# Optimization experiments

Measured on AMD Instinct MI355X. Metric: run time of the kernel, lower is better.

## Reference

```python
import jax, jax.numpy as jnp
import numpy as np

B, LC, LP, D, H = 16, 1024, 1024, 128, 4
PFEAT = 1024  # hardcoded p_param rows in the original module


def _xavier(k, shape, gain=1.414):
    fan_in, fan_out = shape[-2], shape[-1]
    a = gain * np.sqrt(6.0 / (fan_in + fan_out))
    return jax.random.uniform(k, shape, minval=-a, maxval=a, dtype=jnp.float32)


def setup_inputs() -> dict:
    key = jax.random.key(0)
    ks = jax.random.split(key, 24)
    inp = {
        "c": jax.random.normal(ks[0], (B, LC, 1), dtype=jnp.float32),
        "c_mask": jnp.ones((B, LC), dtype=jnp.float32),
        "p": jax.random.normal(ks[1], (B, LP, PFEAT), dtype=jnp.float32),
        "p_mask": jnp.ones((B, LP), dtype=jnp.float32),
        # learned params; linear weights stored as [in, out] (transposed vs torch)
        "c_param": _xavier(ks[2], (1, D)),
        "p_param": _xavier(ks[3], (PFEAT, D)),
        "U": _xavier(ks[4], (H, D, D)),
        "W_p2c": _xavier(ks[5], (H, D, D)),
        "b_p2c": jnp.zeros((H, D), dtype=jnp.float32),
        "W_c2p": _xavier(ks[6], (H, D, D)),
        "b_c2p": jnp.zeros((H, D), dtype=jnp.float32),
        "Wh_c": _xavier(ks[7], (H, D, D)),
        "bh_c": jnp.zeros((H, D), dtype=jnp.float32),
        "Wh_p": _xavier(ks[8], (H, D, D)),
        "bh_p": jnp.zeros((H, D), dtype=jnp.float32),
        "Wa_c": _xavier(ks[9], (H, 2 * D, 1))[..., 0],  # [H, 2D]
        "ba_c": jnp.zeros((H,), dtype=jnp.float32),
        "Wa_p": _xavier(ks[10], (H, 2 * D, 1))[..., 0],
        "ba_p": jnp.zeros((H,), dtype=jnp.float32),
        "W_comb_c": _xavier(ks[11], (H * D, D)),
        "b_comb_c": jnp.zeros((D,), dtype=jnp.float32),
        "W_comb_p": _xavier(ks[12], (H * D, D)),
        "b_comb_p": jnp.zeros((D,), dtype=jnp.float32),
    }
    return inp


def _mask_softmax(a, mask):
    # a, mask broadcastable; softmax over last axis with mask applied post-exp
    a_max = jnp.max(a, axis=-1, keepdims=True)
    e = jnp.exp(a - a_max) * mask
    return e / (jnp.sum(e, axis=-1, keepdims=True) + 1e-6)


def reference(c, c_mask, p, p_mask, c_param, p_param, U, W_p2c, b_p2c,
              W_c2p, b_c2p, Wh_c, bh_c, Wh_p, bh_p, Wa_c, ba_c, Wa_p, ba_p,
              W_comb_c, b_comb_c, W_comb_p, b_comb_p):
    b = c.shape[0]
    cv = jnp.matmul(c, c_param)          # [b, Lc, d]
    pv = jnp.matmul(p, p_param)          # [b, Lp, d]

    # bilinear attention map per head: [b, H, Lc, Lp]
    A = jnp.tanh(jnp.einsum("bld,hde,bme->bhlm", cv, U, pv))
    A = A * (c_mask[:, None, :, None] * p_mask[:, None, None, :])

    pt = jnp.tanh(jnp.einsum("bmd,hde->bhme", pv, W_p2c) + b_p2c[None, :, None, :])
    c_trans = jnp.einsum("bhlm,bhme->bhle", A, pt)      # [b,H,Lc,d]
    ct = jnp.tanh(jnp.einsum("bld,hde->bhle", cv, W_c2p) + b_c2p[None, :, None, :])
    p_trans = jnp.einsum("bhlm,bhle->bhme", A, ct)      # [b,H,Lp,d]

    hc = jnp.tanh(jnp.einsum("bld,hde->bhle", cv, Wh_c) + bh_c[None, :, None, :])
    hp = jnp.tanh(jnp.einsum("bmd,hde->bhme", pv, Wh_p) + bh_p[None, :, None, :])

    # attention logits: linear over concat([hidden, trans]) -> split the weight
    score_c = (jnp.einsum("bhle,he->bhl", hc, Wa_c[:, :128])
               + jnp.einsum("bhle,he->bhl", c_trans, Wa_c[:, 128:])
               + ba_c[None, :, None])
    score_p = (jnp.einsum("bhme,he->bhm", hp, Wa_p[:, :128])
               + jnp.einsum("bhme,he->bhm", p_trans, Wa_p[:, 128:])
               + ba_p[None, :, None])

    c_att = _mask_softmax(score_c, c_mask[:, None, :])  # [b,H,Lc]
    p_att = _mask_softmax(score_p, p_mask[:, None, :])  # [b,H,Lp]

    cf = jnp.einsum("bld,bhl->bhd", cv, c_att).reshape(b, -1)  # [b, H*d]
    pf = jnp.einsum("bmd,bhm->bhd", pv, p_att).reshape(b, -1)

    cf_final = cf @ W_comb_c + b_comb_c  # [b, d]
    pf_final = pf @ W_comb_p + b_comb_p  # [b, d]
    return cf_final[:, :, None] * pf_final[:, None, :]  # [b, d, d]
```

## Files before the change

kernel.cpp:

```cpp
#include <hip/hip_runtime.h>


using bf16x8 = __attribute__((ext_vector_type(8))) short;
using u16x8  = __attribute__((ext_vector_type(8))) unsigned short;
using f32x4  = __attribute__((ext_vector_type(4))) float;

#define TWO_LOG2E 2.8853900817779268f

__device__ __forceinline__ float exp2_raw(float x){
#if __has_builtin(__builtin_amdgcn_exp2f)
  return __builtin_amdgcn_exp2f(x);
#else
  float r; asm("v_exp_f32 %0, %1" : "=v"(r) : "v"(x)); return r;
#endif
}
__device__ __forceinline__ float tanh_fast(float x){
  float e = exp2_raw(x * TWO_LOG2E);
  return fmaf(-2.0f, __builtin_amdgcn_rcpf(e + 1.0f), 1.0f);
}
__device__ __forceinline__ unsigned short f2bf(float f){
  unsigned u = __float_as_uint(f);
  u = (u + 0x7FFFu + ((u >> 16) & 1u)) >> 16;
  return (unsigned short)u;
}
__device__ __forceinline__ float bf2f(unsigned short s){
  return __uint_as_float((unsigned)s << 16);
}
__device__ __forceinline__ unsigned cvt_pk_bf16(float a, float b){
  unsigned r;
  asm("v_cvt_pk_bf16_f32 %0, %1, %2" : "=v"(r) : "v"(a), "v"(b));
  return r;
}
__device__ __forceinline__ void split8(const float4& x, const float4& y, bf16x8& hi, bf16x8& lo){
  unsigned h0 = cvt_pk_bf16(x.x, x.y);
  unsigned h1 = cvt_pk_bf16(x.z, x.w);
  unsigned h2 = cvt_pk_bf16(y.x, y.y);
  unsigned h3 = cvt_pk_bf16(y.z, y.w);
  float r0 = x.x - __uint_as_float(h0 << 16);
  float r1 = x.y - __uint_as_float(h0 & 0xffff0000u);
  float r2 = x.z - __uint_as_float(h1 << 16);
  float r3 = x.w - __uint_as_float(h1 & 0xffff0000u);
  float r4 = y.x - __uint_as_float(h2 << 16);
  float r5 = y.y - __uint_as_float(h2 & 0xffff0000u);
  float r6 = y.z - __uint_as_float(h3 << 16);
  float r7 = y.w - __uint_as_float(h3 & 0xffff0000u);
  uint4 H = make_uint4(h0, h1, h2, h3);
  uint4 L = make_uint4(cvt_pk_bf16(r0, r1), cvt_pk_bf16(r2, r3),
                       cvt_pk_bf16(r4, r5), cvt_pk_bf16(r6, r7));
  hi = __builtin_bit_cast(bf16x8, H);
  lo = __builtin_bit_cast(bf16x8, L);
}

__global__ __launch_bounds__(256) void ka_prep(
    const float* __restrict__ c_param,
    const float* __restrict__ U, const float* __restrict__ W_comb_c,
    const float* __restrict__ Wh_c, const float* __restrict__ W_c2p,
    const float* __restrict__ p_param, const float* __restrict__ W_p2c,
    const float* __restrict__ Wh_p,
    float* __restrict__ uh, float* __restrict__ wccv,
    float* __restrict__ whc_v, float* __restrict__ wc2p_v,
    unsigned short* __restrict__ ppT_hi, unsigned short* __restrict__ ppT_lo,
    unsigned short* __restrict__ wp2cT_hi, unsigned short* __restrict__ wp2cT_lo,
    unsigned short* __restrict__ whpT_hi, unsigned short* __restrict__ whpT_lo)
{
  __shared__ float T[64*68];
  int bid0 = blockIdx.x, t = threadIdx.x;
  if (bid0 < 4) {
    int h = bid0;
    if (t < 128) {
      float s_uh = 0.f, s_wcc = 0.f, s_whc = 0.f, s_wc2p = 0.f;
      for (int d = 0; d < 128; ++d) {
        float cp = c_param[d];
        s_uh   += cp * U[(h*128 + d)*128 + t];
        s_wcc  += cp * W_comb_c[(h*128 + d)*128 + t];
        s_whc  += cp * Wh_c[(h*128 + d)*128 + t];
        s_wc2p += cp * W_c2p[(h*128 + d)*128 + t];
      }
      uh[h*128 + t]     = s_uh;
      wccv[h*128 + t]   = s_wcc;
      whc_v[h*128 + t]  = s_whc;
      wc2p_v[h*128 + t] = s_wc2p;
    }
    return;
  }
  int bid = bid0 - 4;
  const float* src; unsigned short* dh; unsigned short* dl;
  int k0, e0, dpitch, drow0;
  if (bid < 32) {
    k0 = (bid >> 1)*64; e0 = (bid & 1)*64;
    src = p_param; dh = ppT_hi; dl = ppT_lo; dpitch = 1024; drow0 = e0;
  } else if (bid < 48) {
    int w = bid - 32; int h = w >> 2, ki = (w >> 1) & 1, ej = w & 1;
    k0 = ki*64; e0 = ej*64;
    src = W_p2c + h*16384; dh = wp2cT_hi; dl = wp2cT_lo; dpitch = 128;
    drow0 = h*128 + e0;
  } else {
    int w = bid - 48; int h = w >> 2, ki = (w >> 1) & 1, ej = w & 1;
    k0 = ki*64; e0 = ej*64;
    src = Wh_p + h*16384; dh = whpT_hi; dl = whpT_lo; dpitch = 128;
    drow0 = h*128 + e0;
  }
  {
    int r = t >> 2, cs = (t & 3)*4;
    const float* s = src + (k0 + r)*128 + e0 + cs;
    #pragma unroll
    for (int j = 0; j < 4; ++j) {
      float4 v = *(const float4*)(s + j*16);
      *(float4*)&T[r*68 + cs + j*16] = v;
    }
  }
  __syncthreads();
  {
    int e = t >> 2, ks = (t & 3)*16;
    unsigned short hs[16], ls[16];
    #pragma unroll
    for (int j = 0; j < 16; ++j) {
      float v = T[(ks + j)*68 + e];
      unsigned short hh = f2bf(v);
      hs[j] = hh; ls[j] = f2bf(v - bf2f(hh));
    }
    unsigned short* ph = dh + (drow0 + e)*dpitch + k0 + ks;
    unsigned short* pl = dl + (drow0 + e)*dpitch + k0 + ks;
    *(u16x8*)ph       = *(u16x8*)&hs[0];
    *(u16x8*)(ph + 8) = *(u16x8*)&hs[8];
    *(u16x8*)pl       = *(u16x8*)&ls[0];
    *(u16x8*)(pl + 8) = *(u16x8*)&ls[8];
  }
}

__global__ __launch_bounds__(256) void kb_pv_maps(
    const float* __restrict__ p,
    const unsigned short* __restrict__ ppT_hi, const unsigned short* __restrict__ ppT_lo,
    float* __restrict__ pv_part0, float* __restrict__ pv_part1,
    const float* __restrict__ c, const float* __restrict__ c_mask,
    const float* __restrict__ whc_v, const float* __restrict__ wc2p_v,
    const float* __restrict__ bh_c, const float* __restrict__ b_c2p,
    const float* __restrict__ Wa_c, const float* __restrict__ Wa_p,
    const float* __restrict__ ba_c,
    float* __restrict__ score_c, float2* __restrict__ pairP)
{
  __shared__ __align__(16) char smem[36864];
  int bid = blockIdx.x, t = threadIdx.x;
  if (bid < 512) {
    short* Bh = (short*)smem;
    short* Bl = (short*)(smem + 18432);
    int khalf = bid >> 8, rowtile = bid & 255;
    int kbase = khalf * 512;
    int row0 = rowtile * 64;
    float* __restrict__ pvp = khalf ? pv_part1 : pv_part0;
    int w = t >> 6, lane = t & 63;
    int l15 = lane & 15, l4 = lane >> 4;

    int bcol = t >> 1, bkh = (t & 1) * 32;
    const unsigned short* gBh = ppT_hi + bcol*1024 + kbase + bkh;
    const unsigned short* gBl = ppT_lo + bcol*1024 + kbase + bkh;
    short* sBh = &Bh[bcol*72 + bkh];
    short* sBl = &Bl[bcol*72 + bkh];

    const float* gA = p + (row0 + w*16 + l15)*1024 + kbase + l4*8;

    u16x8 rb[8];
    float4 ra[4];

    #pragma unroll
    for (int j = 0; j < 4; ++j) {
      rb[j]   = *(const u16x8*)(gBh + j*8);
      rb[4+j] = *(const u16x8*)(gBl + j*8);
    }
    #pragma unroll
    for (int j = 0; j < 4; ++j)
      ra[j] = *(const float4*)(gA + (j>>1)*32 + (j&1)*4);

    f32x4 acc[8];
    #pragma unroll
    for (int n = 0; n < 8; ++n) acc[n] = (f32x4){0.f,0.f,0.f,0.f};

    for (int kc = 0; kc < 8; ++kc) {
      __syncthreads();
      #pragma unroll
      for (int j = 0; j < 4; ++j) {
        *(u16x8*)(sBh + j*8) = rb[j];
        *(u16x8*)(sBl + j*8) = rb[4+j];
      }
      if (kc < 7) {
        #pragma unroll
        for (int j = 0; j < 4; ++j) {
          rb[j]   = *(const u16x8*)(gBh + (kc+1)*64 + j*8);
          rb[4+j] = *(const u16x8*)(gBl + (kc+1)*64 + j*8);
        }
      }
      float4 ran0, ran1, ran2, ran3;
      if (kc < 7) {
        const float* gAn = gA + (kc+1)*64;
        ran0 = *(const float4*)(gAn);
        ran1 = *(const float4*)(gAn + 4);
        ran2 = *(const float4*)(gAn + 32);
        ran3 = *(const float4*)(gAn + 36);
      }
      __syncthreads();
      #pragma unroll
      for (int ks = 0; ks < 2; ++ks) {
        bf16x8 ah, al;
        split8(ra[2*ks], ra[2*ks+1], ah, al);
        #pragma unroll
        for (int ct = 0; ct < 8; ++ct) {
          bf16x8 bh = *(const bf16x8*)&Bh[(ct*16 + l15)*72 + ks*32 + l4*8];
          bf16x8 bl = *(const bf16x8*)&Bl[(ct*16 + l15)*72 + ks*32 + l4*8];
          acc[ct] = __builtin_amdgcn_mfma_f32_16x16x32_bf16(ah, bh, acc[ct], 0, 0, 0);
          acc[ct] = __builtin_amdgcn_mfma_f32_16x16x32_bf16(ah, bl, acc[ct], 0, 0, 0);
          acc[ct] = __builtin_amdgcn_mfma_f32_16x16x32_bf16(al, bh, acc[ct], 0, 0, 0);
        }
      }
      if (kc < 7) { ra[0] = ran0; ra[1] = ran1; ra[2] = ran2; ra[3] = ran3; }
    }

    #pragma unroll
    for (int ct = 0; ct < 8; ++ct) {
      int col = ct*16 + l15;
      #pragma unroll
      for (int r = 0; r < 4; ++r) {
        int row = row0 + w*16 + l4*4 + r;
        pvp[row*128 + col] = acc[ct][r];
      }
    }
  } else {
    float* fsh = (float*)smem;
    float* whc_l  = fsh;
    float* wc2p_l = fsh + 128;
    float* bhc_l  = fsh + 256;
    float* bc2p_l = fsh + 384;
    float* wac1_l = fsh + 512;
    float* wap2_l = fsh + 640;
    int i = bid - 512;
    int b = i >> 4, h = (i >> 2) & 3, lc = i & 3;
    if (t < 128) {
      whc_l[t]  = whc_v[h*128 + t];
      wc2p_l[t] = wc2p_v[h*128 + t];
      bhc_l[t]  = bh_c[h*128 + t];
      bc2p_l[t] = b_c2p[h*128 + t];
      wac1_l[t] = Wa_c[h*256 + t];
      wap2_l[t] = Wa_p[h*256 + 128 + t];
    }
    __syncthreads();
    int l = lc*256 + t;
    float cl = c[b*1024 + l];
    float a1 = 0.f, a2 = 0.f;
    #pragma unroll 4
    for (int e = 0; e < 128; ++e) {
      a1 += wac1_l[e] * tanh_fast(cl*whc_l[e]  + bhc_l[e]);
      a2 += wap2_l[e] * tanh_fast(cl*wc2p_l[e] + bc2p_l[e]);
    }
    int o = (b*4 + h)*1024 + l;
    score_c[o] = a1 + ba_c[h];
    pairP[o] = make_float2(TWO_LOG2E * cl, c_mask[b*1024 + l] * a2);
  }
}

__global__ __launch_bounds__(256) void kc_head(
    const float* __restrict__ pv0, const float* __restrict__ pv1,
    const unsigned short* __restrict__ wp2cT_hi, const unsigned short* __restrict__ wp2cT_lo,
    const unsigned short* __restrict__ whpT_hi, const unsigned short* __restrict__ whpT_lo,
    const float* __restrict__ b_p2c, const float* __restrict__ bh_p,
    const float* __restrict__ Wa_c, const float* __restrict__ Wa_p,
    const float* __restrict__ p_mask, const float* __restrict__ ba_p,
    const float* __restrict__ uh,
    float2* __restrict__ pairC, float* __restrict__ score_p,
    float* __restrict__ g_arr, float* __restrict__ pv_sum)
{
  __shared__ __align__(16) short Whs[64*136];
  __shared__ __align__(16) short Wls[64*136];
  int t = threadIdx.x;
  int bid = blockIdx.x;
  int ph = bid >> 7, mtile = bid & 127;
  int path = ph >> 2, h = ph & 3;
  int w = t >> 6, lane = t & 63;
  int l15 = lane & 15, l4 = lane >> 4;

  const unsigned short* Wgh = (path ? whpT_hi : wp2cT_hi) + h*16384;
  const unsigned short* Wgl = (path ? whpT_lo : wp2cT_lo) + h*16384;
  int e2 = t >> 2, k0s = (t & 3)*32;

  u16x8 wr_h[4], wr_l[4];
  {
    const u16x8* sh = (const u16x8*)(Wgh + e2*128 + k0s);
    const u16x8* sl = (const u16x8*)(Wgl + e2*128 + k0s);
    #pragma unroll
    for (int j = 0; j < 4; ++j) { wr_h[j] = sh[j]; wr_l[j] = sl[j]; }
  }

  const float* bias_g = path ? bh_p : b_p2c;
  float biasv[8], wav[8];
  #pragma unroll
  for (int n = 0; n < 8; ++n) {
    int col = n*16 + l15;
    biasv[n] = bias_g[h*128 + col];
    wav[n]   = path ? Wa_p[h*256 + col] : Wa_c[h*256 + 128 + col];
  }

  int rowbase = mtile*128 + w*32;
  bf16x8 afh[2][4], afl[2][4];
  float gacc[2] = {0.f, 0.f};
  #pragma unroll
  for (int rtile = 0; rtile < 2; ++rtile) {
    int off = (rowbase + rtile*16 + l15)*128 + l4*8;
    #pragma unroll
    for (int kt = 0; kt < 4; ++kt) {
      float4 x0 = *(const float4*)(pv0 + off + kt*32);
      float4 y0 = *(const float4*)(pv0 + off + kt*32 + 4);
      float4 x1 = *(const float4*)(pv1 + off + kt*32);
      float4 y1 = *(const float4*)(pv1 + off + kt*32 + 4);
      float4 x = make_float4(x0.x+x1.x, x0.y+x1.y, x0.z+x1.z, x0.w+x1.w);
      float4 y = make_float4(y0.x+y1.x, y0.y+y1.y, y0.z+y1.z, y0.w+y1.w);
      if (ph == 0) {
        *(float4*)(pv_sum + off + kt*32)     = x;
        *(float4*)(pv_sum + off + kt*32 + 4) = y;
      }
      split8(x, y, afh[rtile][kt], afl[rtile][kt]);
      if (!path) {
        float4 u0 = *(const float4*)(uh + h*128 + kt*32 + l4*8);
        float4 u1 = *(const float4*)(uh + h*128 + kt*32 + l4*8 + 4);
        gacc[rtile] += x.x*u0.x + x.y*u0.y + x.z*u0.z + x.w*u0.w
                     + y.x*u1.x + y.y*u1.y + y.z*u1.z + y.w*u1.w;
      }
    }
  }
  if (!path) {
    #pragma unroll
    for (int rtile = 0; rtile < 2; ++rtile) {
      float gg = gacc[rtile];
      gg += __shfl_xor(gg, 16, 64);
      gg += __shfl_xor(gg, 32, 64);
      if (l4 == 0) {
        int grow = rowbase + rtile*16 + l15;
        int bb = grow >> 10, m = grow & 1023;
        int idx = (bb*4 + h)*1024 + m;
        g_arr[idx] = gg;
        pairC[idx].x = TWO_LOG2E * gg;
      }
    }
  }

  f32x4 acc[2][8];
  #pragma unroll
  for (int rtile = 0; rtile < 2; ++rtile)
    #pragma unroll
    for (int n = 0; n < 8; ++n) acc[rtile][n] = (f32x4){0.f,0.f,0.f,0.f};

  {
    u16x8* dhh = (u16x8*)&Whs[e2*136 + k0s];
    u16x8* dll = (u16x8*)&Wls[e2*136 + k0s];
    #pragma unroll
    for (int j = 0; j < 4; ++j) { dhh[j] = wr_h[j]; dll[j] = wr_l[j]; }
  }
  __syncthreads();

  {
    const u16x8* sh = (const u16x8*)(Wgh + (64 + e2)*128 + k0s);
    const u16x8* sl = (const u16x8*)(Wgl + (64 + e2)*128 + k0s);
    #pragma unroll
    for (int j = 0; j < 4; ++j) { wr_h[j] = sh[j]; wr_l[j] = sl[j]; }
  }

  #pragma unroll
  for (int n = 0; n < 4; ++n) {
    #pragma unroll
    for (int kt = 0; kt < 4; ++kt) {
      bf16x8 bh = *(const bf16x8*)&Whs[(n*16 + l15)*136 + kt*32 + l4*8];
      bf16x8 bl = *(const bf16x8*)&Wls[(n*16 + l15)*136 + kt*32 + l4*8];
      #pragma unroll
      for (int rtile = 0; rtile < 2; ++rtile) {
        acc[rtile][n] = __builtin_amdgcn_mfma_f32_16x16x32_bf16(afh[rtile][kt], bh, acc[rtile][n], 0, 0, 0);
        acc[rtile][n] = __builtin_amdgcn_mfma_f32_16x16x32_bf16(afh[rtile][kt], bl, acc[rtile][n], 0, 0, 0);
        acc[rtile][n] = __builtin_amdgcn_mfma_f32_16x16x32_bf16(afl[rtile][kt], bh, acc[rtile][n], 0, 0, 0);
      }
    }
  }
  __syncthreads();
  {
    u16x8* dhh = (u16x8*)&Whs[e2*136 + k0s];
    u16x8* dll = (u16x8*)&Wls[e2*136 + k0s];
    #pragma unroll
    for (int j = 0; j < 4; ++j) { dhh[j] = wr_h[j]; dll[j] = wr_l[j]; }
  }
  __syncthreads();
  #pragma unroll
  for (int n = 0; n < 4; ++n) {
    int nn = 4 + n;
    #pragma unroll
    for (int kt = 0; kt < 4; ++kt) {
      bf16x8 bh = *(const bf16x8*)&Whs[(n*16 + l15)*136 + kt*32 + l4*8];
      bf16x8 bl = *(const bf16x8*)&Wls[(n*16 + l15)*136 + kt*32 + l4*8];
      #pragma unroll
      for (int rtile = 0; rtile < 2; ++rtile) {
        acc[rtile][nn] = __builtin_amdgcn_mfma_f32_16x16x32_bf16(afh[rtile][kt], bh, acc[rtile][nn], 0, 0, 0);
        acc[rtile][nn] = __builtin_amdgcn_mfma_f32_16x16x32_bf16(afh[rtile][kt], bl, acc[rtile][nn], 0, 0, 0);
        acc[rtile][nn] = __builtin_amdgcn_mfma_f32_16x16x32_bf16(afl[rtile][kt], bh, acc[rtile][nn], 0, 0, 0);
      }
    }
  }

  #pragma unroll
  for (int rtile = 0; rtile < 2; ++rtile) {
    float pp0 = 0.f, pp1 = 0.f, pp2 = 0.f, pp3 = 0.f;
    #pragma unroll
    for (int n = 0; n < 8; ++n) {
      float bb = biasv[n], ww = wav[n];
      pp0 += ww * tanh_fast(acc[rtile][n][0] + bb);
      pp1 += ww * tanh_fast(acc[rtile][n][1] + bb);
      pp2 += ww * tanh_fast(acc[rtile][n][2] + bb);
      pp3 += ww * tanh_fast(acc[rtile][n][3] + bb);
    }
    #pragma unroll
    for (int off = 1; off < 16; off <<= 1) {
      pp0 += __shfl_xor(pp0, off, 64);
      pp1 += __shfl_xor(pp1, off, 64);
      pp2 += __shfl_xor(pp2, off, 64);
      pp3 += __shfl_xor(pp3, off, 64);
    }
    if (l15 == 0) {
      int grow = rowbase + rtile*16 + l4*4;
      int bb = grow >> 10, m = grow & 1023;
      int idx = (bb*4 + h)*1024 + m;
      if (path) {
        float bap = ba_p[h];
        *(float4*)&score_p[idx] = make_float4(pp0+bap, pp1+bap, pp2+bap, pp3+bap);
      } else {
        float4 mk = *(const float4*)&p_mask[bb*1024 + m];
        pairC[idx+0].y = mk.x * pp0;
        pairC[idx+1].y = mk.y * pp1;
        pairC[idx+2].y = mk.z * pp2;
        pairC[idx+3].y = mk.w * pp3;
      }
    }
  }
}

__global__ __launch_bounds__(256) void kd_scores(
    const float* __restrict__ c, const float* __restrict__ c_mask, const float* __restrict__ p_mask,
    const float* __restrict__ g_arr,
    const float2* __restrict__ pairC, const float2* __restrict__ pairP,
    float* __restrict__ score_c, float* __restrict__ score_p)
{
  __shared__ float2 pr[256];
  __shared__ float red[4];
  int bid = blockIdx.x, t = threadIdx.x;
  int side = bid >> 9;
  int r = bid & 511;
  int b = r >> 5, h = (r >> 3) & 3, ac = (r >> 2) & 1, jc = r & 3;
  int bh = b*4 + h;
  const float2* pair = (side ? pairP : pairC) + bh*1024 + jc*256;

  float2 mine = pair[t];
  pr[t] = mine;
  float partB = mine.y;
  #pragma unroll
  for (int off = 1; off < 64; off <<= 1) partB += __shfl_xor(partB, off, 64);
  if ((t & 63) == 0) red[t >> 6] = partB;

  int ai1 = ac*512 + t, ai2 = ai1 + 256;
  float alpha1, alpha2, mask1, mask2;
  if (side) {
    alpha1 = g_arr[bh*1024 + ai1]; alpha2 = g_arr[bh*1024 + ai2];
    mask1  = p_mask[b*1024 + ai1]; mask2  = p_mask[b*1024 + ai2];
  } else {
    alpha1 = c[b*1024 + ai1]; alpha2 = c[b*1024 + ai2];
    mask1  = c_mask[b*1024 + ai1]; mask2  = c_mask[b*1024 + ai2];
  }
  __syncthreads();
  float sB = red[0] + red[1] + red[2] + red[3];

  float acc1 = 0.f, acc2 = 0.f;
  #pragma unroll 8
  for (int j = 0; j < 256; ++j) {
    float2 gb = pr[j];
    float e1 = exp2_raw(alpha1 * gb.x);
    float e2 = exp2_raw(alpha2 * gb.x);
    acc1 = fmaf(gb.y, __builtin_amdgcn_rcpf(e1 + 1.0f), acc1);
    acc2 = fmaf(gb.y, __builtin_amdgcn_rcpf(e2 + 1.0f), acc2);
  }
  float* sc = side ? score_p : score_c;
  atomicAdd(sc + bh*1024 + ai1, mask1 * (sB - 2.0f*acc1));
  atomicAdd(sc + bh*1024 + ai2, mask2 * (sB - 2.0f*acc2));
}

__device__ __forceinline__ float blk_red_max(float v, float* red, int t){
  red[t] = v; __syncthreads();
  for (int s = 128; s; s >>= 1) { if (t < s) red[t] = fmaxf(red[t], red[t+s]); __syncthreads(); }
  float r = red[0]; __syncthreads();
  return r;
}
__device__ __forceinline__ float blk_red_sum(float v, float* red, int t){
  red[t] = v; __syncthreads();
  for (int s = 128; s; s >>= 1) { if (t < s) red[t] += red[t+s]; __syncthreads(); }
  float r = red[0]; __syncthreads();
  return r;
}

__global__ __launch_bounds__(256) void ke_soft(
    const float* __restrict__ c, const float* __restrict__ c_mask, const float* __restrict__ p_mask,
    const float* __restrict__ score_c, const float* __restrict__ score_p,
    const float* __restrict__ pv_sum,
    float* __restrict__ s_c, float* __restrict__ pf_pool)
{
  __shared__ float sv[1024];
  __shared__ float red[256];
  int bid = blockIdx.x, t = threadIdx.x;
  bool sideP = bid >= 64;
  int i = bid & 63;
  int b = i >> 2, h = i & 3, bh = b*4 + h;
  const float* sc = (sideP ? score_p : score_c) + bh*1024;
  const float* mk = (sideP ? p_mask : c_mask) + b*1024;

  float v[4];
  float mx = -1e30f;
  #pragma unroll
  for (int j = 0; j < 4; ++j) { v[j] = sc[t + j*256]; mx = fmaxf(mx, v[j]); }
  mx = blk_red_max(mx, red, t);
  float sum = 0.f;
  #pragma unroll
  for (int j = 0; j < 4; ++j) {
    float e = exp2_raw((v[j] - mx) * 1.4426950408889634f) * mk[t + j*256];
    sv[t + j*256] = e;
    sum += e;
  }
  sum = blk_red_sum(sum, red, t);
  float rinv = __fdividef(1.0f, sum + 1e-6f);

  if (!sideP) {
    float a = 0.f;
    #pragma unroll
    for (int j = 0; j < 4; ++j) a += sv[t + j*256] * rinv * c[b*1024 + t + j*256];
    a = blk_red_sum(a, red, t);
    if (t == 0) s_c[bh] = a;
  } else {
    #pragma unroll
    for (int j = 0; j < 4; ++j) sv[t + j*256] *= rinv;
    __syncthreads();
    int e = t & 127, half = t >> 7;
    float acc = 0.f;
    const float* base = pv_sum + (b*1024 + half*512)*128 + e;
    #pragma unroll 4
    for (int m = 0; m < 512; ++m) acc += sv[half*512 + m] * base[m*128];
    red[t] = acc; __syncthreads();
    if (t < 128) pf_pool[bh*128 + t] = red[t] + red[t + 128];
  }
}

__global__ __launch_bounds__(256) void kf_final(
    const float* __restrict__ s_c, const float* __restrict__ wccv,
    const float* __restrict__ b_comb_c, const float* __restrict__ pf_pool,
    const float* __restrict__ W_comb_p, const float* __restrict__ b_comb_p,
    float* __restrict__ out)
{
  __shared__ float pfr[512];
  __shared__ float cfl[128], pfl[128];
  int b = blockIdx.x, t = threadIdx.x;
  pfr[t]       = pf_pool[b*512 + t];
  pfr[t + 256] = pf_pool[b*512 + t + 256];
  __syncthreads();
  if (t < 128) {
    float cf = b_comb_c[t];
    #pragma unroll
    for (int h = 0; h < 4; ++h) cf += s_c[b*4 + h] * wccv[h*128 + t];
    float pf = b_comb_p[t];
    #pragma unroll 8
    for (int i = 0; i < 512; ++i) pf += pfr[i] * W_comb_p[i*128 + t];
    cfl[t] = cf; pfl[t] = pf;
  }
  __syncthreads();
  #pragma unroll
  for (int k = 0; k < 64; ++k) {
    int idx = k*256 + t;
    out[b*16384 + idx] = cfl[idx >> 7] * pfl[idx & 127];
  }
}

extern "C" void kernel_launch(void* const* d_in, const int* in_sizes, int n_in,
                              void* d_out, int out_size, void* d_ws, size_t ws_size,
                              hipStream_t stream)
{
  const float* c        = (const float*)d_in[0];
  const float* c_mask   = (const float*)d_in[1];
  const float* p        = (const float*)d_in[2];
  const float* p_mask   = (const float*)d_in[3];
  const float* c_param  = (const float*)d_in[4];
  const float* p_param  = (const float*)d_in[5];
  const float* U        = (const float*)d_in[6];
  const float* W_p2c    = (const float*)d_in[7];
  const float* b_p2c    = (const float*)d_in[8];
  const float* W_c2p    = (const float*)d_in[9];
  const float* b_c2p    = (const float*)d_in[10];
  const float* Wh_c     = (const float*)d_in[11];
  const float* bh_c     = (const float*)d_in[12];
  const float* Wh_p     = (const float*)d_in[13];
  const float* bh_p     = (const float*)d_in[14];
  const float* Wa_c     = (const float*)d_in[15];
  const float* ba_c     = (const float*)d_in[16];
  const float* Wa_p     = (const float*)d_in[17];
  const float* ba_p     = (const float*)d_in[18];
  const float* W_comb_c = (const float*)d_in[19];
  const float* b_comb_c = (const float*)d_in[20];
  const float* W_comb_p = (const float*)d_in[21];
  const float* b_comb_p = (const float*)d_in[22];
  float* out = (float*)d_out;

  char* ws = (char*)d_ws;
  float*          pv_part0 = (float*)         (ws + 0);
  float*          pv_part1 = (float*)         (ws + 8388608);
  float*          pv_sum   = (float*)         (ws + 16777216);
  unsigned short* ppT_hi   = (unsigned short*)(ws + 25165824);
  unsigned short* ppT_lo   = (unsigned short*)(ws + 25427968);
  unsigned short* wp2cT_hi = (unsigned short*)(ws + 25690112);
  unsigned short* wp2cT_lo = (unsigned short*)(ws + 25821184);
  unsigned short* whpT_hi  = (unsigned short*)(ws + 25952256);
  unsigned short* whpT_lo  = (unsigned short*)(ws + 26083328);
  float*          uh       = (float*)         (ws + 26214400);
  float*          wccv     = (float*)         (ws + 26216448);
  float*          whc_v    = (float*)         (ws + 26218496);
  float*          wc2p_v   = (float*)         (ws + 26220544);
  float*          g_arr    = (float*)         (ws + 26222592);
  float2*         pairC    = (float2*)        (ws + 26484736);
  float2*         pairP    = (float2*)        (ws + 27009024);
  float*          score_c  = (float*)         (ws + 27533312);
  float*          score_p  = (float*)         (ws + 27795456);
  float*          s_c      = (float*)         (ws + 28057600);
  float*          pf_pool  = (float*)         (ws + 28057856);

  ka_prep<<<dim3(68), dim3(256), 0, stream>>>(
      c_param, U, W_comb_c, Wh_c, W_c2p, p_param, W_p2c, Wh_p,
      uh, wccv, whc_v, wc2p_v,
      ppT_hi, ppT_lo, wp2cT_hi, wp2cT_lo, whpT_hi, whpT_lo);

  kb_pv_maps<<<dim3(768), dim3(256), 0, stream>>>(
      p, ppT_hi, ppT_lo, pv_part0, pv_part1,
      c, c_mask, whc_v, wc2p_v, bh_c, b_c2p, Wa_c, Wa_p, ba_c,
      score_c, pairP);

  kc_head<<<dim3(1024), dim3(256), 0, stream>>>(
      pv_part0, pv_part1, wp2cT_hi, wp2cT_lo, whpT_hi, whpT_lo,
      b_p2c, bh_p, Wa_c, Wa_p, p_mask, ba_p, uh, pairC, score_p, g_arr, pv_sum);

  kd_scores<<<dim3(1024), dim3(256), 0, stream>>>(
      c, c_mask, p_mask, g_arr, pairC, pairP, score_c, score_p);

  ke_soft<<<dim3(128), dim3(256), 0, stream>>>(
      c, c_mask, p_mask, score_c, score_p, pv_sum, s_c, pf_pool);

  kf_final<<<dim3(16), dim3(256), 0, stream>>>(
      s_c, wccv, b_comb_c, pf_pool, W_comb_p, b_comb_p, out);
}
```

Before: 150.5 us.

## Share tanh tiles between both score directions and split p-side pooling across blocks

```diff
diff --git a/kernel.cpp b/kernel.cpp
--- a/kernel.cpp
+++ b/kernel.cpp
@@ -436,51 +436,57 @@
 }
 
 __global__ __launch_bounds__(256) void kd_scores(
-    const float* __restrict__ c, const float* __restrict__ c_mask, const float* __restrict__ p_mask,
+    const float* __restrict__ c_mask, const float* __restrict__ p_mask,
     const float* __restrict__ g_arr,
     const float2* __restrict__ pairC, const float2* __restrict__ pairP,
     float* __restrict__ score_c, float* __restrict__ score_p)
 {
-  __shared__ float2 pr[256];
-  __shared__ float red[4];
+  __shared__ float T[128*65];
+  __shared__ float gm_s[64], ptw_s[64], pm_s[64];
+  __shared__ float kl_s[128], ctw_s[128], cm_s[128];
   int bid = blockIdx.x, t = threadIdx.x;
-  int side = bid >> 9;
-  int r = bid & 511;
-  int b = r >> 5, h = (r >> 3) & 3, ac = (r >> 2) & 1, jc = r & 3;
-  int bh = b*4 + h;
-  const float2* pair = (side ? pairP : pairC) + bh*1024 + jc*256;
-
-  float2 mine = pair[t];
-  pr[t] = mine;
-  float partB = mine.y;
-  #pragma unroll
-  for (int off = 1; off < 64; off <<= 1) partB += __shfl_xor(partB, off, 64);
-  if ((t & 63) == 0) red[t >> 6] = partB;
-
-  int ai1 = ac*512 + t, ai2 = ai1 + 256;
-  float alpha1, alpha2, mask1, mask2;
-  if (side) {
-    alpha1 = g_arr[bh*1024 + ai1]; alpha2 = g_arr[bh*1024 + ai2];
-    mask1  = p_mask[b*1024 + ai1]; mask2  = p_mask[b*1024 + ai2];
-  } else {
-    alpha1 = c[b*1024 + ai1]; alpha2 = c[b*1024 + ai2];
-    mask1  = c_mask[b*1024 + ai1]; mask2  = c_mask[b*1024 + ai2];
-  }
-  __syncthreads();
-  float sB = red[0] + red[1] + red[2] + red[3];
-
-  float acc1 = 0.f, acc2 = 0.f;
-  #pragma unroll 8
-  for (int j = 0; j < 256; ++j) {
-    float2 gb = pr[j];
-    float e1 = exp2_raw(alpha1 * gb.x);
-    float e2 = exp2_raw(alpha2 * gb.x);
-    acc1 = fmaf(gb.y, __builtin_amdgcn_rcpf(e1 + 1.0f), acc1);
-    acc2 = fmaf(gb.y, __builtin_amdgcn_rcpf(e2 + 1.0f), acc2);
-  }
-  float* sc = side ? score_p : score_c;
-  atomicAdd(sc + bh*1024 + ai1, mask1 * (sB - 2.0f*acc1));
-  atomicAdd(sc + bh*1024 + ai2, mask2 * (sB - 2.0f*acc2));
+  int bh = bid >> 7, tile = bid & 127;
+  int b = bh >> 2;
+  int l0 = (tile >> 4) * 128, m0 = (tile & 15) * 64;
+  if (t < 64) {
+    gm_s[t]  = g_arr[bh*1024 + m0 + t];
+    ptw_s[t] = pairC[bh*1024 + m0 + t].y;
+    pm_s[t]  = p_mask[b*1024 + m0 + t];
+  } else if (t < 192) {
+    int l = t - 64;
+    float2 pp = pairP[bh*1024 + l0 + l];
+    kl_s[l] = pp.x; ctw_s[l] = pp.y;
+    cm_s[l] = c_mask[b*1024 + l0 + l];
+  }
+  __syncthreads();
+  {
+    int r = t >> 1, hm = t & 1;
+    float kl = kl_s[r];
+    float accc = 0.f;
+    #pragma unroll 8
+    for (int j = 0; j < 32; ++j) {
+      int m = hm*32 + j;
+      float e = exp2_raw(kl * gm_s[m]);
+      float tt = fmaf(-2.0f, __builtin_amdgcn_rcpf(e + 1.0f), 1.0f);
+      T[r*65 + m] = tt;
+      accc = fmaf(ptw_s[m], tt, accc);
+    }
+    accc += __shfl_xor(accc, 1, 64);
+    if (hm == 0) atomicAdd(score_c + bh*1024 + l0 + r, cm_s[r]*accc);
+  }
+  __syncthreads();
+  {
+    int col = t >> 2, q = t & 3;
+    float accp = 0.f;
+    #pragma unroll 8
+    for (int j = 0; j < 32; ++j) {
+      int l = q*32 + j;
+      accp = fmaf(ctw_s[l], T[l*65 + col], accp);
+    }
+    accp += __shfl_xor(accp, 1, 64);
+    accp += __shfl_xor(accp, 2, 64);
+    if (q == 0) atomicAdd(score_p + bh*1024 + m0 + col, pm_s[col]*accp);
+  }
 }
 
 __device__ __forceinline__ float blk_red_max(float v, float* red, int t){
@@ -500,63 +506,79 @@
     const float* __restrict__ c, const float* __restrict__ c_mask, const float* __restrict__ p_mask,
     const float* __restrict__ score_c, const float* __restrict__ score_p,
     const float* __restrict__ pv_sum,
-    float* __restrict__ s_c, float* __restrict__ pf_pool)
+    float* __restrict__ s_c, float* __restrict__ pf_part)
 {
   __shared__ float sv[1024];
   __shared__ float red[256];
   int bid = blockIdx.x, t = threadIdx.x;
-  bool sideP = bid >= 64;
-  int i = bid & 63;
-  int b = i >> 2, h = i & 3, bh = b*4 + h;
-  const float* sc = (sideP ? score_p : score_c) + bh*1024;
-  const float* mk = (sideP ? p_mask : c_mask) + b*1024;
-
-  float v[4];
-  float mx = -1e30f;
-  #pragma unroll
-  for (int j = 0; j < 4; ++j) { v[j] = sc[t + j*256]; mx = fmaxf(mx, v[j]); }
-  mx = blk_red_max(mx, red, t);
-  float sum = 0.f;
-  #pragma unroll
-  for (int j = 0; j < 4; ++j) {
-    float e = exp2_raw((v[j] - mx) * 1.4426950408889634f) * mk[t + j*256];
-    sv[t + j*256] = e;
-    sum += e;
-  }
-  sum = blk_red_sum(sum, red, t);
-  float rinv = __fdividef(1.0f, sum + 1e-6f);
-
-  if (!sideP) {
+  if (bid < 64) {
+    int b = bid >> 2, h = bid & 3, bh = b*4 + h;
+    const float* sc = score_c + bh*1024;
+    const float* mk = c_mask + b*1024;
+    float v[4];
+    float mx = -1e30f;
+    #pragma unroll
+    for (int j = 0; j < 4; ++j) { v[j] = sc[t + j*256]; mx = fmaxf(mx, v[j]); }
+    mx = blk_red_max(mx, red, t);
+    float sum = 0.f;
+    #pragma unroll
+    for (int j = 0; j < 4; ++j) {
+      float e = exp2_raw((v[j] - mx) * 1.4426950408889634f) * mk[t + j*256];
+      sv[t + j*256] = e;
+      sum += e;
+    }
+    sum = blk_red_sum(sum, red, t);
+    float rinv = __fdividef(1.0f, sum + 1e-6f);
     float a = 0.f;
     #pragma unroll
     for (int j = 0; j < 4; ++j) a += sv[t + j*256] * rinv * c[b*1024 + t + j*256];
     a = blk_red_sum(a, red, t);
     if (t == 0) s_c[bh] = a;
   } else {
-    #pragma unroll
-    for (int j = 0; j < 4; ++j) sv[t + j*256] *= rinv;
-    __syncthreads();
-    int e = t & 127, half = t >> 7;
+    int i = bid - 64;
+    int b = i >> 4, h = (i >> 2) & 3, ch = i & 3, bh = b*4 + h;
+    const float* sc = score_p + bh*1024;
+    const float* mk = p_mask + b*1024;
+    float v[4];
+    float mx = -1e30f;
+    #pragma unroll
+    for (int j = 0; j < 4; ++j) { v[j] = sc[t + j*256]; mx = fmaxf(mx, v[j]); }
+    mx = blk_red_max(mx, red, t);
+    float sum = 0.f;
+    #pragma unroll
+    for (int j = 0; j < 4; ++j) {
+      float e = exp2_raw((v[j] - mx) * 1.4426950408889634f) * mk[t + j*256];
+      sv[t + j*256] = e;
+      sum += e;
+    }
+    sum = blk_red_sum(sum, red, t);
+    float rinv = __fdividef(1.0f, sum + 1e-6f);
+    int e0 = t & 127, seg = t >> 7;
+    int mbase = ch*256 + seg*128;
     float acc = 0.f;
-    const float* base = pv_sum + (b*1024 + half*512)*128 + e;
+    const float* base = pv_sum + (b*1024 + mbase)*128 + e0;
     #pragma unroll 4
-    for (int m = 0; m < 512; ++m) acc += sv[half*512 + m] * base[m*128];
+    for (int m = 0; m < 128; ++m) acc = fmaf(sv[mbase + m]*rinv, base[m*128], acc);
     red[t] = acc; __syncthreads();
-    if (t < 128) pf_pool[bh*128 + t] = red[t] + red[t + 128];
+    if (t < 128) pf_part[(ch*16 + b)*512 + h*128 + t] = red[t] + red[t + 128];
   }
 }
 
 __global__ __launch_bounds__(256) void kf_final(
     const float* __restrict__ s_c, const float* __restrict__ wccv,
-    const float* __restrict__ b_comb_c, const float* __restrict__ pf_pool,
+    const float* __restrict__ b_comb_c, const float* __restrict__ pf_part,
     const float* __restrict__ W_comb_p, const float* __restrict__ b_comb_p,
     float* __restrict__ out)
 {
   __shared__ float pfr[512];
   __shared__ float cfl[128], pfl[128];
   int b = blockIdx.x, t = threadIdx.x;
-  pfr[t]       = pf_pool[b*512 + t];
-  pfr[t + 256] = pf_pool[b*512 + t + 256];
+  #pragma unroll
+  for (int s = 0; s < 2; ++s) {
+    int idx = t + s*256;
+    pfr[idx] = pf_part[(0*16 + b)*512 + idx] + pf_part[(1*16 + b)*512 + idx]
+             + pf_part[(2*16 + b)*512 + idx] + pf_part[(3*16 + b)*512 + idx];
+  }
   __syncthreads();
   if (t < 128) {
     float cf = b_comb_c[t];
@@ -624,7 +646,7 @@
   float*          score_c  = (float*)         (ws + 27533312);
   float*          score_p  = (float*)         (ws + 27795456);
   float*          s_c      = (float*)         (ws + 28057600);
-  float*          pf_pool  = (float*)         (ws + 28057856);
+  float*          pf_part  = (float*)         (ws + 28057856);
 
   ka_prep<<<dim3(68), dim3(256), 0, stream>>>(
       c_param, U, W_comb_c, Wh_c, W_c2p, p_param, W_p2c, Wh_p,
@@ -640,12 +662,12 @@
       pv_part0, pv_part1, wp2cT_hi, wp2cT_lo, whpT_hi, whpT_lo,
       b_p2c, bh_p, Wa_c, Wa_p, p_mask, ba_p, uh, pairC, score_p, g_arr, pv_sum);
 
-  kd_scores<<<dim3(1024), dim3(256), 0, stream>>>(
-      c, c_mask, p_mask, g_arr, pairC, pairP, score_c, score_p);
-
-  ke_soft<<<dim3(128), dim3(256), 0, stream>>>(
-      c, c_mask, p_mask, score_c, score_p, pv_sum, s_c, pf_pool);
+  kd_scores<<<dim3(8192), dim3(256), 0, stream>>>(
+      c_mask, p_mask, g_arr, pairC, pairP, score_c, score_p);
+
+  ke_soft<<<dim3(320), dim3(256), 0, stream>>>(
+      c, c_mask, p_mask, score_c, score_p, pv_sum, s_c, pf_part);
 
   kf_final<<<dim3(16), dim3(256), 0, stream>>>(
-      s_c, wccv, b_comb_c, pf_pool, W_comb_p, b_comb_p, out);
-}
+      s_c, wccv, b_comb_c, pf_part, W_comb_p, b_comb_p, out);
+}
```

New measurement: 132.9 us. 1.13x faster.
